# Kernel tuning notes

Hardware: AMD Instinct MI355X
Metric: run time of the kernel (lower is better)

Reference implementation:

```python
import jax, jax.numpy as jnp
import numpy as np

FH, FW = 38, 50          # stride-16 feature map of a 608x800 image
N_ROIS = 512
SCALE = 1.0 / 16.0
R = 7                    # roi_size -> 7x7 position-sensitive bins, 2x2 crop per bin
OUT_DIM = 10


def _conv(x, w, b, pad):
    # NCHW conv, stride 1, asymmetric 'same' padding for (k,1)/(1,k) kernels
    y = jax.lax.conv_general_dilated(
        x, w, (1, 1), [(pad[0], pad[0]), (pad[1], pad[1])],
        dimension_numbers=('NCHW', 'OIHW', 'NCHW'))
    return y + b[None, :, None, None]


def setup_inputs() -> dict:
    key = jax.random.key(0)
    ks = jax.random.split(key, 20)
    x = jax.random.normal(ks[0], (1, 2048, FH, FW), jnp.float32)
    # rois: unnormalized [x1,y1,x2,y2] in image coordinates, strictly inside the image
    img_h, img_w = FH * 16.0, FW * 16.0
    u = jax.random.uniform(ks[1], (N_ROIS, 4))
    x1 = u[:, 0] * (img_w * 0.5)
    y1 = u[:, 1] * (img_h * 0.5)
    x2 = x1 + 16.0 + u[:, 2] * (img_w - 17.0 - x1)
    y2 = y1 + 16.0 + u[:, 3] * (img_h - 17.0 - y1)
    rois = jnp.stack([x1, y1, x2, y2], axis=1)
    std = 0.01  # normal_init(0, 0.01)
    p = lambda k, shape: jax.random.normal(k, shape, jnp.float32) * std
    inp = {
        'x': x, 'rois': rois,
        'w_col_max': p(ks[2], (256, 2048, 15, 1)), 'b_col_max': jnp.zeros((256,), jnp.float32),
        'w_col':     p(ks[3], (490, 256, 1, 15)),  'b_col':     jnp.zeros((490,), jnp.float32),
        'w_row_max': p(ks[4], (256, 2048, 1, 15)), 'b_row_max': jnp.zeros((256,), jnp.float32),
        'w_row':     p(ks[5], (490, 256, 15, 1)),  'b_row':     jnp.zeros((490,), jnp.float32),
        'w_fc1':   p(ks[6], (2048, 490)), 'b_fc1':   jnp.zeros((2048,), jnp.float32),
        'w_score': p(ks[7], (81, 2048)),  'b_score': jnp.zeros((81,), jnp.float32),
        'w_loc':   p(ks[8], (324, 2048)), 'b_loc':   jnp.zeros((324,), jnp.float32),
    }
    return inp


def reference(x, rois, w_col_max, b_col_max, w_col, b_col,
              w_row_max, b_row_max, w_row, b_row,
              w_fc1, b_fc1, w_score, b_score, w_loc, b_loc):
    # ---- GlobalContextModule: large separable 15-tap convs ----
    h_col = _conv(_conv(x, w_col_max, b_col_max, (7, 0)), w_col, b_col, (0, 7))
    h_row = _conv(_conv(x, w_row_max, b_row_max, (0, 7)), w_row, b_row, (7, 0))
    h = jax.nn.relu(h_col + h_row)  # [1, 490, H, W]
    H, W = h.shape[2], h.shape[3]

    # ---- position-sensitive crop-and-resize + per-bin max, fully vectorized ----
    b = rois * SCALE / jnp.array([W, H, W, H], jnp.float32)  # normalized [x1,y1,x2,y2]
    xmin, ymin, xmax, ymax = b[:, 0], b[:, 1], b[:, 2], b[:, 3]
    step_x = (xmax - xmin) / R
    step_y = (ymax - ymin) / R
    # sample offsets: bin index (0..R-1) + crop sample (0 or 1); crop size 2 => samples at bin edges
    g = jnp.arange(R, dtype=jnp.float32)[None, :, None] + jnp.arange(2, dtype=jnp.float32)[None, None, :]
    ys = (ymin[:, None, None] + g * step_y[:, None, None]) * (H - 1)  # [N, R, 2]
    xs = (xmin[:, None, None] + g * step_x[:, None, None]) * (W - 1)  # [N, R, 2]

    def idx_w(v, vmax):
        v0 = jnp.floor(v)
        f = v - v0
        i0 = jnp.clip(v0, 0, vmax - 1).astype(jnp.int32)
        i1 = jnp.clip(v0 + 1.0, 0, vmax - 1).astype(jnp.int32)
        return i0, i1, f

    yi0, yi1, wy = idx_w(ys, H)
    xi0, xi1, wx = idx_w(xs, W)

    feat = h[0].reshape(R * R, OUT_DIM, H, W).transpose(0, 2, 3, 1)  # [49, H, W, 10]
    bidx = (jnp.arange(R)[:, None] * R + jnp.arange(R)[None, :])[None, :, :, None, None]  # [1,R,R,1,1]
    Y0 = yi0[:, :, None, :, None]; Y1 = yi1[:, :, None, :, None]  # [N,R,1,2,1]
    X0 = xi0[:, None, :, None, :]; X1 = xi1[:, None, :, None, :]  # [N,1,R,1,2]
    WY = wy[:, :, None, :, None, None]
    WX = wx[:, None, :, None, :, None]

    v00 = feat[bidx, Y0, X0]; v01 = feat[bidx, Y0, X1]
    v10 = feat[bidx, Y1, X0]; v11 = feat[bidx, Y1, X1]  # [N,R,R,2,2,10]
    top = v00 + (v01 - v00) * WX
    bot = v10 + (v11 - v10) * WX
    val = top + (bot - top) * WY
    pooled = val.max(axis=(3, 4))                       # [N, R, R, 10]
    flat = pooled.reshape(pooled.shape[0], -1)          # [N, 490], order = bin*10 + c

    fc1 = jax.nn.relu(flat @ w_fc1.T + b_fc1)           # [N, 2048]
    roi_cls_locs = fc1 @ w_loc.T + b_loc                # [N, 324]
    roi_scores = fc1 @ w_score.T + b_score              # [N, 81]
    return roi_cls_locs, roi_scores
```

## Files before the change

### kernel.cpp

```cpp
#include <hip/hip_runtime.h>
#include <math.h>

#define FW 50
#define FH 38
#define NPIX 1900
#define NROIS 512

#define CSH 2470
#define CSV 2650

typedef __bf16 bf16x8 __attribute__((ext_vector_type(8)));
typedef float  f32x4  __attribute__((ext_vector_type(4)));
typedef float  f32x16 __attribute__((ext_vector_type(16)));

__device__ __forceinline__ unsigned short f2b(float f) {
    unsigned int u = __float_as_uint(f);
    unsigned int r = (u + 0x7fffu + ((u >> 16) & 1u)) >> 16;
    return (unsigned short)r;
}


__global__ __launch_bounds__(256) void zero_us(unsigned short* __restrict__ p, int n) {
    int i = (blockIdx.x * 256 + threadIdx.x) * 8;
    if (i < n) { uint4 z; z.x = z.y = z.z = z.w = 0u; *(uint4*)(p + i) = z; }
}

__global__ __launch_bounds__(256) void cvt_bf16(
    const float* __restrict__ in, unsigned short* __restrict__ out, int n)
{
    int i = (blockIdx.x * 256 + threadIdx.x) * 4;
    if (i >= n) return;
    float4 v = *(const float4*)(in + i);
    ushort2 a, b;
    a.x = f2b(v.x); a.y = f2b(v.y);
    b.x = f2b(v.z); b.y = f2b(v.w);
    *(ushort2*)(out + i)     = a;
    *(ushort2*)(out + i + 2) = b;
}

__global__ __launch_bounds__(256) void cvt_pad(
    const float* __restrict__ in, unsigned short* __restrict__ out,
    int rows, int Kin, int Kout)
{
    int idx = blockIdx.x * 256 + threadIdx.x;
    if (idx >= rows * Kout) return;
    int rw = idx / Kout, k = idx - rw * Kout;
    out[idx] = (k < Kin) ? f2b(in[(size_t)rw * Kin + k]) : (unsigned short)0;
}

__global__ __launch_bounds__(256) void repack_w(
    const float* __restrict__ w, unsigned short* __restrict__ out, int n)
{
    int idx = blockIdx.x * 256 + threadIdx.x;
    if (idx >= n) return;
    int t = idx & 15;
    int oc = idx >> 4;
    out[idx] = (t < 15) ? f2b(w[oc * 15 + t]) : (unsigned short)0;
}

__global__ __launch_bounds__(256) void xpad_h(
    const float* __restrict__ xs, unsigned short* __restrict__ out)
{
    int idx = blockIdx.x * 256 + threadIdx.x;
    if (idx >= 2048 * CSH) return;
    int c = idx / CSH;
    int rem = idx - c * CSH;
    int y = rem / 65;
    int xc = rem - y * 65 - 7;
    unsigned short v = 0;
    if (xc >= 0 && xc < FW) v = f2b(xs[(c * FH + y) * FW + xc]);
    out[idx] = v;
}

__global__ __launch_bounds__(256) void xpad_v(
    const float* __restrict__ xs, unsigned short* __restrict__ out)
{
    int idx = blockIdx.x * 256 + threadIdx.x;
    if (idx >= 2048 * CSV) return;
    int c = idx / CSV;
    int rem = idx - c * CSV;
    int xx = rem / 53;
    int yc = rem - xx * 53 - 7;
    unsigned short v = 0;
    if (yc >= 0 && yc < FH) v = f2b(xs[(c * FH + yc) * FW + xx]);
    out[idx] = v;
}

__global__ __launch_bounds__(256) void conv_tap(
    const unsigned short* __restrict__ Wt,
    const unsigned short* __restrict__ Xp,
    float* __restrict__ P,
    int M, int Kp, int Mpad, int CS, int yMul, int xMul,
    int zMask, int zBits, int yMask, int xShift)
{
    const int id = blockIdx.x;
    const int zt = id & zMask;
    const int yt = (id >> zBits) & yMask;
    const int xt = id >> xShift;
    const int nsplit = zMask + 1;

    const int Ks = Kp / nsplit;
    const int k0 = zt * Ks;
    const int tid  = threadIdx.x;
    const int lane = tid & 63;
    const int wave = tid >> 6;
    const int mbase = yt * 128;
    const int pbase = xt * 128;

    __shared__ unsigned short As[2][128][40];
    __shared__ unsigned short Bt[2][128][40];

    const int a_row = tid >> 1;
    const int a_k16 = (tid & 1) << 4;
    const int a_src = min(mbase + a_row, M - 1);
    const unsigned short* Abase = Wt + (size_t)a_src * Kp + a_k16;

    const int b_pix = tid >> 1;
    const int bh    = tid & 1;
    int p = pbase + b_pix;
    if (p > NPIX - 1) p = NPIX - 1;
    const int py = p / FW, px = p - py * FW;
    const int pixBase = py * yMul + px * xMul;
    const unsigned* __restrict__ Bdw = (const unsigned*)Xp;

    f32x16 acc[2][2];
#pragma unroll
    for (int i = 0; i < 2; ++i)
#pragma unroll
        for (int j = 0; j < 2; ++j)
#pragma unroll
            for (int r = 0; r < 16; ++r) acc[i][j][r] = 0.f;

    const int wy = (wave >> 1) * 64;
    const int wx = (wave & 1) * 64;
    const int l5 = lane & 31;
    const int l8 = (lane >> 5) * 8;

    uint4 aR0, aR1;
    unsigned d[9];

    auto loadA = [&](int kt) {
        aR0 = *(const uint4*)(Abase + kt);
        aR1 = *(const uint4*)(Abase + kt + 8);
    };
    auto loadB = [&](int kt) {
        const int cg = (kt >> 4) + bh;
        const unsigned base = ((unsigned)(cg * CS + pixBase)) >> 1;
#pragma unroll
        for (int j = 0; j < 9; ++j) d[j] = Bdw[base + j];
    };

    loadA(k0); loadB(k0);
    const unsigned sh = ((unsigned)(pixBase & 1)) << 4;

    int buf = 0;
    for (int kt = k0; kt < k0 + Ks; kt += 32) {
        unsigned ob[8];
#pragma unroll
        for (int j = 0; j < 8; ++j)
            ob[j] = __builtin_amdgcn_alignbit(d[j + 1], d[j], sh);
        *(uint4*)&As[buf][a_row][a_k16]     = aR0;
        *(uint4*)&As[buf][a_row][a_k16 + 8] = aR1;
        *(uint4*)&Bt[buf][b_pix][bh * 16]     = *(uint4*)&ob[0];
        *(uint4*)&Bt[buf][b_pix][bh * 16 + 8] = *(uint4*)&ob[4];
        __syncthreads();

        if (kt + 32 < k0 + Ks) { loadA(kt + 32); loadB(kt + 32); }

        bf16x8 af[2][2], bfr[2][2];
#pragma unroll
        for (int i = 0; i < 2; ++i)
#pragma unroll
            for (int kk = 0; kk < 2; ++kk) {
                af[i][kk]  = __builtin_bit_cast(bf16x8,
                    *(const uint4*)&As[buf][wy + i * 32 + l5][kk * 16 + l8]);
                bfr[i][kk] = __builtin_bit_cast(bf16x8,
                    *(const uint4*)&Bt[buf][wx + i * 32 + l5][kk * 16 + l8]);
            }
#pragma unroll
        for (int kk = 0; kk < 2; ++kk)
#pragma unroll
            for (int i = 0; i < 2; ++i)
#pragma unroll
                for (int j = 0; j < 2; ++j)
                    acc[i][j] = __builtin_amdgcn_mfma_f32_32x32x16_bf16(
                        af[i][kk], bfr[j][kk], acc[i][j], 0, 0, 0);
        buf ^= 1;
    }

    float* Pp = P + (size_t)zt * Mpad * NPIX;
#pragma unroll
    for (int i = 0; i < 2; ++i) {
        const int mb = mbase + wy + i * 32 + (lane >> 5) * 4;
#pragma unroll
        for (int j = 0; j < 2; ++j) {
            const int pp = pbase + wx + j * 32 + l5;
            if (pp < NPIX) {
#pragma unroll
                for (int r = 0; r < 16; ++r) {
                    const int m = mb + (r & 3) + 8 * (r >> 2);
                    Pp[(size_t)m * NPIX + pp] = acc[i][j][r];
                }
            }
        }
    }
}

__global__ void reduce_pad(
    const float* __restrict__ P, int Mpad, int nsplit,
    const float* __restrict__ bias, int M,
    unsigned short* __restrict__ outb, int CS, int yMul, int xMul)
{
    int idx = blockIdx.x * 256 + threadIdx.x;
    if (idx >= M * NPIX) return;
    int o = idx / NPIX;
    int p = idx - o * NPIX;
    float s = bias[o];
    for (int sp = 0; sp < nsplit; ++sp)
        s += P[((size_t)sp * Mpad + o) * NPIX + p];
    int y = p / FW, x = p - y * FW;
    outb[(size_t)o * CS + y * yMul + x * xMul + 7] = f2b(s);
}

__global__ void reduce_bias(
    const float* __restrict__ P, int Mpad, int nsplit,
    const float* __restrict__ bias, int M,
    const float* __restrict__ addbuf, int relu,
    float* __restrict__ outf)
{
    int idx = blockIdx.x * blockDim.x + threadIdx.x;
    if (idx >= M * NPIX) return;
    int o = idx / NPIX;
    int p = idx - o * NPIX;
    float s = bias[o];
    for (int sp = 0; sp < nsplit; ++sp)
        s += P[((size_t)sp * Mpad + o) * NPIX + p];
    if (addbuf) s += addbuf[idx];
    if (relu) s = fmaxf(s, 0.f);
    outf[idx] = s;
}

__global__ __launch_bounds__(512) void pool_kernel(
    const float* __restrict__ h, const float* __restrict__ rois,
    unsigned short* __restrict__ pooledb)
{
    int n = blockIdx.x;
    int k = threadIdx.x;
    if (k >= 490) {
        pooledb[(size_t)n * 512 + k] = 0;
        return;
    }
    float x1 = rois[n * 4 + 0], y1 = rois[n * 4 + 1];
    float x2 = rois[n * 4 + 2], y2 = rois[n * 4 + 3];
    float xmin = x1 * (1.f / 16.f) / 50.f;
    float ymin = y1 * (1.f / 16.f) / 38.f;
    float xmax = x2 * (1.f / 16.f) / 50.f;
    float ymax = y2 * (1.f / 16.f) / 38.f;
    float step_x = (xmax - xmin) / 7.f;
    float step_y = (ymax - ymin) / 7.f;
    int bin = k / 10;
    int bi = bin / 7, bj = bin - bi * 7;
    const float* ch = h + (size_t)k * NPIX;
    float m = -INFINITY;
#pragma unroll
    for (int sy = 0; sy < 2; ++sy) {
        float yv = (ymin + (float)(bi + sy) * step_y) * 37.f;
        float y0 = floorf(yv);
        float fy = yv - y0;
        int yi0 = min(max((int)y0, 0), 37);
        int yi1 = min(max((int)y0 + 1, 0), 37);
#pragma unroll
        for (int sx = 0; sx < 2; ++sx) {
            float xv = (xmin + (float)(bj + sx) * step_x) * 49.f;
            float x0 = floorf(xv);
            float fx = xv - x0;
            int xi0 = min(max((int)x0, 0), 49);
            int xi1 = min(max((int)x0 + 1, 0), 49);
            float v00 = ch[yi0 * FW + xi0], v01 = ch[yi0 * FW + xi1];
            float v10 = ch[yi1 * FW + xi0], v11 = ch[yi1 * FW + xi1];
            float top = v00 + (v01 - v00) * fx;
            float bot = v10 + (v11 - v10) * fx;
            float val = top + (bot - top) * fy;
            m = fmaxf(m, val);
        }
    }
    pooledb[(size_t)n * 512 + k] = f2b(m);
}

__global__ __launch_bounds__(256) void fc_mfma(
    const unsigned short* __restrict__ Wb,
    const unsigned short* __restrict__ Act,
    float* __restrict__ P, int M, int Kld, int Mpad)
{
    const int Ks = Kld / gridDim.z;
    const int k0 = blockIdx.z * Ks;
    const int tid  = threadIdx.x;
    const int lane = tid & 63;
    const int wave = tid >> 6;
    const int mbase = blockIdx.x * 64;
    const int nbase = blockIdx.y * 64;

    __shared__ unsigned short As[64][40];
    __shared__ unsigned short Bs[64][40];

    const int s_r  = tid >> 2;
    const int s_k8 = (tid & 3) << 3;
    const int a_row = mbase + s_r;
    const bool a_ok = a_row < M;
    const unsigned short* Abase = Wb + (size_t)a_row * Kld + s_k8;
    const unsigned short* Bbase = Act + (size_t)(nbase + s_r) * Kld + s_k8;

    f32x4 acc[2][2];
#pragma unroll
    for (int i = 0; i < 2; ++i)
#pragma unroll
        for (int j = 0; j < 2; ++j)
#pragma unroll
            for (int r = 0; r < 4; ++r) acc[i][j][r] = 0.f;

    const int mh = (wave >> 1) * 32;
    const int nh = (wave & 1) * 32;
    const int lm = lane & 15;
    const int l8 = (lane >> 4) * 8;

    uint4 aReg, bReg;
    if (a_ok) aReg = *(const uint4*)(Abase + k0);
    else { aReg.x = aReg.y = aReg.z = aReg.w = 0u; }
    bReg = *(const uint4*)(Bbase + k0);

    for (int kt = k0; kt < k0 + Ks; kt += 32) {
        *(uint4*)&As[s_r][s_k8] = aReg;
        *(uint4*)&Bs[s_r][s_k8] = bReg;
        __syncthreads();

        if (kt + 32 < k0 + Ks) {
            if (a_ok) aReg = *(const uint4*)(Abase + kt + 32);
            bReg = *(const uint4*)(Bbase + kt + 32);
        }

        bf16x8 a0 = __builtin_bit_cast(bf16x8, *(const uint4*)&As[mh + lm][l8]);
        bf16x8 a1 = __builtin_bit_cast(bf16x8, *(const uint4*)&As[mh + 16 + lm][l8]);
        bf16x8 b0 = __builtin_bit_cast(bf16x8, *(const uint4*)&Bs[nh + lm][l8]);
        bf16x8 b1 = __builtin_bit_cast(bf16x8, *(const uint4*)&Bs[nh + 16 + lm][l8]);

        acc[0][0] = __builtin_amdgcn_mfma_f32_16x16x32_bf16(a0, b0, acc[0][0], 0, 0, 0);
        acc[0][1] = __builtin_amdgcn_mfma_f32_16x16x32_bf16(a0, b1, acc[0][1], 0, 0, 0);
        acc[1][0] = __builtin_amdgcn_mfma_f32_16x16x32_bf16(a1, b0, acc[1][0], 0, 0, 0);
        acc[1][1] = __builtin_amdgcn_mfma_f32_16x16x32_bf16(a1, b1, acc[1][1], 0, 0, 0);
        __syncthreads();
    }

#pragma unroll
    for (int ms = 0; ms < 2; ++ms)
#pragma unroll
        for (int ns = 0; ns < 2; ++ns) {
            int n  = nbase + nh + ns * 16 + lm;
            int m0 = mbase + mh + ms * 16 + (lane >> 4) * 4;
            float* Pp = P + ((size_t)blockIdx.z * NROIS + n) * Mpad + m0;
            *(f32x4*)Pp = acc[ms][ns];
        }
}

__global__ void fc_reduce(
    const float* __restrict__ P, int Mpad, int M, int nsplit,
    const float* __restrict__ bias, int relu,
    float* __restrict__ outf, unsigned short* __restrict__ outb)
{
    int idx = blockIdx.x * 256 + threadIdx.x;
    if (idx >= NROIS * M) return;
    int n = idx / M, m = idx - n * M;
    float s = bias[m];
    for (int sp = 0; sp < nsplit; ++sp)
        s += P[((size_t)sp * NROIS + n) * Mpad + m];
    if (relu) s = fmaxf(s, 0.f);
    if (outf) outf[idx] = s;
    if (outb) outb[idx] = f2b(s);
}

extern "C" void kernel_launch(void* const* d_in, const int* in_sizes, int n_in,
                              void* d_out, int out_size, void* d_ws, size_t ws_size,
                              hipStream_t stream) {
    const float* x         = (const float*)d_in[0];
    const float* rois      = (const float*)d_in[1];
    const float* w_col_max = (const float*)d_in[2];
    const float* b_col_max = (const float*)d_in[3];
    const float* w_col     = (const float*)d_in[4];
    const float* b_col     = (const float*)d_in[5];
    const float* w_row_max = (const float*)d_in[6];
    const float* b_row_max = (const float*)d_in[7];
    const float* w_row     = (const float*)d_in[8];
    const float* b_row     = (const float*)d_in[9];
    const float* w_fc1     = (const float*)d_in[10];
    const float* b_fc1     = (const float*)d_in[11];
    const float* w_score   = (const float*)d_in[12];
    const float* b_score   = (const float*)d_in[13];
    const float* w_loc     = (const float*)d_in[14];
    const float* b_loc     = (const float*)d_in[15];

    float* part = (float*)d_ws;
    unsigned short* XvU   = (unsigned short*)(part + 7782400);
    unsigned short* XhU   = XvU + 5427264;
    unsigned short* wbig  = XhU + 5058624;
    unsigned short* wc16  = wbig + 8388608;
    unsigned short* wr16  = wc16 + 2007040;
    unsigned short* c1colb= wr16 + 2007040;
    unsigned short* c1rowb= c1colb + 632384;
    unsigned short* wfc1b = c1rowb + 678464;
    unsigned short* pooledb = wfc1b + 1048576;
    unsigned short* fc1b  = pooledb + 262144;
    unsigned short* wlocb = fc1b + 1048576;
    unsigned short* wscoreb = wlocb + 663552;
    float* hcol = (float*)XvU;
    float* h    = (float*)XhU;

    xpad_v<<<21200, 256, 0, stream>>>(x, XvU);
    xpad_h<<<19760, 256, 0, stream>>>(x, XhU);
    zero_us<<<641, 256, 0, stream>>>(c1colb, 1310848);
    repack_w<<<32768, 256, 0, stream>>>(w_col_max, wbig, 8388608);
    repack_w<<<7840, 256, 0, stream>>>(w_col, wc16, 2007040);
    repack_w<<<7840, 256, 0, stream>>>(w_row, wr16, 2007040);
    cvt_pad <<<4096, 256, 0, stream>>>(w_fc1, wfc1b, 2048, 490, 512);
    cvt_bf16<<<648,  256, 0, stream>>>(w_loc, wlocb, 663552);
    cvt_bf16<<<162,  256, 0, stream>>>(w_score, wscoreb, 165888);

    conv_tap<<<480, 256, 0, stream>>>(wbig, XvU, part, 256, 32768, 256, CSV, 1, 53, 15, 4, 1, 5);
    reduce_pad<<<1900, 256, 0, stream>>>(part, 256, 16, b_col_max, 256, c1colb, CSH, 65, 1);
    repack_w<<<32768, 256, 0, stream>>>(w_row_max, wbig, 8388608);
    conv_tap<<<480, 256, 0, stream>>>(wbig, XhU, part, 256, 32768, 256, CSH, 65, 1, 15, 4, 1, 5);
    reduce_pad<<<1900, 256, 0, stream>>>(part, 256, 16, b_row_max, 256, c1rowb, CSV, 1, 53);

    conv_tap<<<480, 256, 0, stream>>>(wc16, c1colb, part, 490, 4096, 512, CSH, 65, 1, 7, 3, 3, 5);
    reduce_bias<<<3637, 256, 0, stream>>>(part, 512, 8, b_col, 490, nullptr, 0, hcol);
    conv_tap<<<480, 256, 0, stream>>>(wr16, c1rowb, part, 490, 4096, 512, CSV, 1, 53, 7, 3, 3, 5);
    reduce_bias<<<3637, 256, 0, stream>>>(part, 512, 8, b_row, 490, hcol, 1, h);

    pool_kernel<<<512, 512, 0, stream>>>(h, rois, pooledb);

    float* out = (float*)d_out;
    fc_mfma<<<dim3(32, 8, 2), 256, 0, stream>>>(wfc1b, pooledb, part, 2048, 512, 2048);
    fc_reduce<<<4096, 256, 0, stream>>>(part, 2048, 2048, 2, b_fc1, 1, nullptr, fc1b);
    fc_mfma<<<dim3(6, 8, 4), 256, 0, stream>>>(wlocb, fc1b, part, 324, 2048, 384);
    fc_reduce<<<648, 256, 0, stream>>>(part, 384, 324, 4, b_loc, 0, out, nullptr);
    fc_mfma<<<dim3(2, 8, 8), 256, 0, stream>>>(wscoreb, fc1b, part, 81, 2048, 128);
    fc_reduce<<<162, 256, 0, stream>>>(part, 128, 81, 8, b_score, 0, out + 512 * 324, nullptr);
}
```

Before: 423.0 us.

## Batch col and row conv branches into dual-launch kernels

Merges the independent column and row convolution branches into single launches with twice the grid. Each half of the grid selects its own weights, input and partial buffer, which fills more CUs per launch than 480 blocks did. The final reduce now sums both partial buffers and applies ReLU in one pass, removing the intermediate hcol write and read. The cost is a second partial buffer and a second repacked weight buffer in the workspace, so the memory footprint grows.

Result: faster. 392.8 us (-7.2%).

```diff
diff --git a/kernel.cpp b/kernel.cpp
--- a/kernel.cpp
+++ b/kernel.cpp
@@ -86,14 +86,23 @@
     out[idx] = v;
 }
 
-__global__ __launch_bounds__(256) void conv_tap(
-    const unsigned short* __restrict__ Wt,
-    const unsigned short* __restrict__ Xp,
-    float* __restrict__ P,
-    int M, int Kp, int Mpad, int CS, int yMul, int xMul,
-    int zMask, int zBits, int yMask, int xShift)
-{
-    const int id = blockIdx.x;
+__global__ __launch_bounds__(256) void conv_dual(
+    const unsigned short* __restrict__ W0, const unsigned short* __restrict__ X0,
+    float* __restrict__ P0, int CS0, int yMul0, int xMul0,
+    const unsigned short* __restrict__ W1, const unsigned short* __restrict__ X1,
+    float* __restrict__ P1, int CS1, int yMul1, int xMul1,
+    int M, int Kp, int Mpad,
+    int zMask, int zBits, int yMask, int xShift, int halfGrid)
+{
+    int id = blockIdx.x;
+    const unsigned short* Wt; const unsigned short* Xp; float* P;
+    int CS, yMul, xMul;
+    if (id < halfGrid) {
+        Wt = W0; Xp = X0; P = P0; CS = CS0; yMul = yMul0; xMul = xMul0;
+    } else {
+        id -= halfGrid;
+        Wt = W1; Xp = X1; P = P1; CS = CS1; yMul = yMul1; xMul = xMul1;
+    }
     const int zt = id & zMask;
     const int yt = (id >> zBits) & yMask;
     const int xt = id >> xShift;
@@ -206,12 +215,19 @@
     }
 }
 
-__global__ void reduce_pad(
-    const float* __restrict__ P, int Mpad, int nsplit,
-    const float* __restrict__ bias, int M,
-    unsigned short* __restrict__ outb, int CS, int yMul, int xMul)
-{
-    int idx = blockIdx.x * 256 + threadIdx.x;
+__global__ void reduce_pad_dual(
+    const float* __restrict__ P0, const float* __restrict__ bias0,
+    unsigned short* __restrict__ out0, int CS0, int yM0, int xM0,
+    const float* __restrict__ P1, const float* __restrict__ bias1,
+    unsigned short* __restrict__ out1, int CS1, int yM1, int xM1,
+    int Mpad, int nsplit, int M, int halfGrid)
+{
+    int b = blockIdx.x;
+    const float* P; const float* bias; unsigned short* outb;
+    int CS, yMul, xMul;
+    if (b < halfGrid) { P = P0; bias = bias0; outb = out0; CS = CS0; yMul = yM0; xMul = xM0; }
+    else { b -= halfGrid; P = P1; bias = bias1; outb = out1; CS = CS1; yMul = yM1; xMul = xM1; }
+    int idx = b * 256 + threadIdx.x;
     if (idx >= M * NPIX) return;
     int o = idx / NPIX;
     int p = idx - o * NPIX;
@@ -222,21 +238,22 @@
     outb[(size_t)o * CS + y * yMul + x * xMul + 7] = f2b(s);
 }
 
-__global__ void reduce_bias(
-    const float* __restrict__ P, int Mpad, int nsplit,
-    const float* __restrict__ bias, int M,
-    const float* __restrict__ addbuf, int relu,
-    float* __restrict__ outf)
-{
-    int idx = blockIdx.x * blockDim.x + threadIdx.x;
+__global__ void reduce_bias_dual(
+    const float* __restrict__ P0, const float* __restrict__ P1,
+    int Mpad, int nsplit,
+    const float* __restrict__ bias0, const float* __restrict__ bias1,
+    int M, float* __restrict__ outf)
+{
+    int idx = blockIdx.x * 256 + threadIdx.x;
     if (idx >= M * NPIX) return;
     int o = idx / NPIX;
     int p = idx - o * NPIX;
-    float s = bias[o];
-    for (int sp = 0; sp < nsplit; ++sp)
-        s += P[((size_t)sp * Mpad + o) * NPIX + p];
-    if (addbuf) s += addbuf[idx];
-    if (relu) s = fmaxf(s, 0.f);
+    float s = bias0[o] + bias1[o];
+    for (int sp = 0; sp < nsplit; ++sp) {
+        s += P0[((size_t)sp * Mpad + o) * NPIX + p];
+        s += P1[((size_t)sp * Mpad + o) * NPIX + p];
+    }
+    s = fmaxf(s, 0.f);
     outf[idx] = s;
 }
 
@@ -397,11 +414,13 @@
     const float* w_loc     = (const float*)d_in[14];
     const float* b_loc     = (const float*)d_in[15];
 
-    float* part = (float*)d_ws;
-    unsigned short* XvU   = (unsigned short*)(part + 7782400);
+    float* part0 = (float*)d_ws;
+    float* part1 = part0 + 7782400;
+    unsigned short* XvU   = (unsigned short*)(part1 + 7782400);
     unsigned short* XhU   = XvU + 5427264;
-    unsigned short* wbig  = XhU + 5058624;
-    unsigned short* wc16  = wbig + 8388608;
+    unsigned short* wbig0 = XhU + 5058624;
+    unsigned short* wbig1 = wbig0 + 8388608;
+    unsigned short* wc16  = wbig1 + 8388608;
     unsigned short* wr16  = wc16 + 2007040;
     unsigned short* c1colb= wr16 + 2007040;
     unsigned short* c1rowb= c1colb + 632384;
@@ -410,37 +429,42 @@
     unsigned short* fc1b  = pooledb + 262144;
     unsigned short* wlocb = fc1b + 1048576;
     unsigned short* wscoreb = wlocb + 663552;
-    float* hcol = (float*)XvU;
-    float* h    = (float*)XhU;
+    float* h = (float*)XhU;
 
     xpad_v<<<21200, 256, 0, stream>>>(x, XvU);
     xpad_h<<<19760, 256, 0, stream>>>(x, XhU);
     zero_us<<<641, 256, 0, stream>>>(c1colb, 1310848);
-    repack_w<<<32768, 256, 0, stream>>>(w_col_max, wbig, 8388608);
+    repack_w<<<32768, 256, 0, stream>>>(w_col_max, wbig0, 8388608);
+    repack_w<<<32768, 256, 0, stream>>>(w_row_max, wbig1, 8388608);
     repack_w<<<7840, 256, 0, stream>>>(w_col, wc16, 2007040);
     repack_w<<<7840, 256, 0, stream>>>(w_row, wr16, 2007040);
     cvt_pad <<<4096, 256, 0, stream>>>(w_fc1, wfc1b, 2048, 490, 512);
     cvt_bf16<<<648,  256, 0, stream>>>(w_loc, wlocb, 663552);
     cvt_bf16<<<162,  256, 0, stream>>>(w_score, wscoreb, 165888);
 
-    conv_tap<<<480, 256, 0, stream>>>(wbig, XvU, part, 256, 32768, 256, CSV, 1, 53, 15, 4, 1, 5);
-    reduce_pad<<<1900, 256, 0, stream>>>(part, 256, 16, b_col_max, 256, c1colb, CSH, 65, 1);
-    repack_w<<<32768, 256, 0, stream>>>(w_row_max, wbig, 8388608);
-    conv_tap<<<480, 256, 0, stream>>>(wbig, XhU, part, 256, 32768, 256, CSH, 65, 1, 15, 4, 1, 5);
-    reduce_pad<<<1900, 256, 0, stream>>>(part, 256, 16, b_row_max, 256, c1rowb, CSV, 1, 53);
-
-    conv_tap<<<480, 256, 0, stream>>>(wc16, c1colb, part, 490, 4096, 512, CSH, 65, 1, 7, 3, 3, 5);
-    reduce_bias<<<3637, 256, 0, stream>>>(part, 512, 8, b_col, 490, nullptr, 0, hcol);
-    conv_tap<<<480, 256, 0, stream>>>(wr16, c1rowb, part, 490, 4096, 512, CSV, 1, 53, 7, 3, 3, 5);
-    reduce_bias<<<3637, 256, 0, stream>>>(part, 512, 8, b_row, 490, hcol, 1, h);
+    conv_dual<<<960, 256, 0, stream>>>(
+        wbig0, XvU, part0, CSV, 1, 53,
+        wbig1, XhU, part1, CSH, 65, 1,
+        256, 32768, 256, 15, 4, 1, 5, 480);
+    reduce_pad_dual<<<3800, 256, 0, stream>>>(
+        part0, b_col_max, c1colb, CSH, 65, 1,
+        part1, b_row_max, c1rowb, CSV, 1, 53,
+        256, 16, 256, 1900);
+
+    conv_dual<<<960, 256, 0, stream>>>(
+        wc16, c1colb, part0, CSH, 65, 1,
+        wr16, c1rowb, part1, CSV, 1, 53,
+        490, 4096, 512, 7, 3, 3, 5, 480);
+    reduce_bias_dual<<<3637, 256, 0, stream>>>(
+        part0, part1, 512, 8, b_col, b_row, 490, h);
 
     pool_kernel<<<512, 512, 0, stream>>>(h, rois, pooledb);
 
     float* out = (float*)d_out;
-    fc_mfma<<<dim3(32, 8, 2), 256, 0, stream>>>(wfc1b, pooledb, part, 2048, 512, 2048);
-    fc_reduce<<<4096, 256, 0, stream>>>(part, 2048, 2048, 2, b_fc1, 1, nullptr, fc1b);
-    fc_mfma<<<dim3(6, 8, 4), 256, 0, stream>>>(wlocb, fc1b, part, 324, 2048, 384);
-    fc_reduce<<<648, 256, 0, stream>>>(part, 384, 324, 4, b_loc, 0, out, nullptr);
-    fc_mfma<<<dim3(2, 8, 8), 256, 0, stream>>>(wscoreb, fc1b, part, 81, 2048, 128);
-    fc_reduce<<<162, 256, 0, stream>>>(part, 128, 81, 8, b_score, 0, out + 512 * 324, nullptr);
-}
+    fc_mfma<<<dim3(32, 8, 2), 256, 0, stream>>>(wfc1b, pooledb, part0, 2048, 512, 2048);
+    fc_reduce<<<4096, 256, 0, stream>>>(part0, 2048, 2048, 2, b_fc1, 1, nullptr, fc1b);
+    fc_mfma<<<dim3(6, 8, 4), 256, 0, stream>>>(wlocb, fc1b, part0, 324, 2048, 384);
+    fc_reduce<<<648, 256, 0, stream>>>(part0, 384, 324, 4, b_loc, 0, out, nullptr);
+    fc_mfma<<<dim3(2, 8, 8), 256, 0, stream>>>(wscoreb, fc1b, part0, 81, 2048, 128);
+    fc_reduce<<<162, 256, 0, stream>>>(part0, 128, 81, 8, b_score, 0, out + 512 * 324, nullptr);
+}
```
